# Kernel optimization log

Hardware: AMD Instinct MI355X
Metric: run time of the kernel (lower is better)

The kernel has to match this reference:

```python
import jax, jax.numpy as jnp
import numpy as np

B, D, H = 2048, 64, 512  # batch, state dim, vf hidden dim
IS_DIFFUSION = True      # vf output divided by 2.0 as in CNF.forward


def setup_inputs() -> dict:
    key = jax.random.key(0)
    ks = jax.random.split(key, 8)

    def lin(k, fi, fo):
        return jax.random.normal(k, (fi, fo), jnp.float32) / np.float32(np.sqrt(fi))

    return {
        "t": jax.random.uniform(ks[0], (1,), jnp.float32),      # scalar time, kept as [1]
        "x": jax.random.normal(ks[1], (B, D + 1), jnp.float32),  # last col = logp channel
        "W1": lin(ks[2], D + 1, H),
        "b1": jax.random.normal(ks[3], (H,), jnp.float32) * 0.01,
        "W2": lin(ks[4], H, H),
        "b2": jax.random.normal(ks[5], (H,), jnp.float32) * 0.01,
        "W3": lin(ks[6], H, D),
        "b3": jax.random.normal(ks[7], (D,), jnp.float32) * 0.01,
    }


def reference(t, x, W1, b1, W2, b2, W3, b3):
    scale = 2.0 if IS_DIFFUSION else 1.0
    xd = x[..., :-1]  # [B, D] -- drop augmented log-density channel

    def vf_single(xi):  # R^D -> R^D vector field, t and params closed over
        h = jnp.concatenate([xi, t])           # [D+1] (time-conditioned input)
        h = jnp.tanh(h @ W1 + b1)
        h = jnp.tanh(h @ W2 + b2)
        return (h @ W3 + b3) / scale

    dx = jax.vmap(vf_single)(xd)  # [B, D]
    # exact divergence: trace of per-sample Jacobian via reverse-mode (matches torch jacrev)
    div = jax.vmap(lambda xi: jnp.trace(jax.jacrev(vf_single)(xi)))(xd)  # [B]
    return jnp.concatenate([dx, div[:, None]], axis=-1)  # [B, D+1]
```

## Files before the change

### kernel.cpp

```cpp
#include <hip/hip_runtime.h>


constexpr int HD = 512;
constexpr int DD = 64;
constexpr int SB = 8;
constexpr int NB = 2048 / SB;

typedef __attribute__((ext_vector_type(8))) short bf16x8;
typedef __attribute__((ext_vector_type(4))) float f32x4;

__device__ inline unsigned short f2bf(float f) {
    union { float f; unsigned u; } v; v.f = f;
    return (unsigned short)((v.u + 0x7fffu + ((v.u >> 16) & 1u)) >> 16);
}
__device__ inline float fast_tanh(float xx) {
    float e = __expf(2.f * xx);
    return 1.f - 2.f / (e + 1.f);
}

__global__ __launch_bounds__(64) void cnf_pack_kernel(
    const float* __restrict__ W1, const float* __restrict__ W2,
    const float* __restrict__ W3, unsigned short* __restrict__ Bpack)
{
    __shared__ float w1s[64][33];
    __shared__ float w3s[16][65];
    const int b = blockIdx.x;
    const int mat = b >> 9, t = (b >> 4) & 31, kk = b & 15;
    const int l = threadIdx.x;
    const int q = l >> 4, nl = l & 15;
    const int n = t * 16 + nl;
    unsigned short o[8];
    if (mat == 0) {
#pragma unroll
        for (int j = 0; j < 8; ++j) {
            int k = kk * 32 + q * 8 + j;
            o[j] = f2bf(W2[k * HD + n]);
        }
    } else {
        for (int e = l; e < 64 * 32; e += 64) {
            int i = e >> 5, kl = e & 31;
            w1s[i][kl] = W1[i * HD + kk * 32 + kl];
        }
        for (int e = l; e < 16 * 64; e += 64) {
            int nn = e >> 6, i = e & 63;
            w3s[nn][i] = W3[(t * 16 + nn) * DD + i];
        }
        __syncthreads();
#pragma unroll
        for (int j = 0; j < 8; ++j) {
            int kl = q * 8 + j;
            float m = 0.f;
#pragma unroll 8
            for (int i = 0; i < 64; ++i) m += w1s[i][kl] * w3s[nl][i];
            o[j] = f2bf(W2[(kk * 32 + kl) * HD + n] * m);
        }
    }
    uint4 pk;
    pk.x = (unsigned)o[0] | ((unsigned)o[1] << 16);
    pk.y = (unsigned)o[2] | ((unsigned)o[3] << 16);
    pk.z = (unsigned)o[4] | ((unsigned)o[5] << 16);
    pk.w = (unsigned)o[6] | ((unsigned)o[7] << 16);
    reinterpret_cast<uint4*>(Bpack)[b * 64 + l] = pk;
}

__global__ __launch_bounds__(512) void cnf_fused_kernel(
    const float* __restrict__ tptr, const float* __restrict__ x,
    const float* __restrict__ W1, const float* __restrict__ b1,
    const float* __restrict__ b2v, const float* __restrict__ W3,
    const float* __restrict__ b3, const unsigned short* __restrict__ Bpack,
    float* __restrict__ out)
{
    __shared__ float4 xsv[65 * 2];
    __shared__ unsigned short A_lds[16][520];
    __shared__ float4 h2v[HD * 2];
    __shared__ float4 divred[8][2];
    __shared__ float sm_b2[HD];

    const int tid  = threadIdx.x;
    const int s0   = blockIdx.x * SB;
    const int wave = tid >> 6, lane = tid & 63;

    {
        const float tval = tptr[0];
        for (int e = tid; e < SB * 65; e += 512) {
            int s = e / 65, i = e % 65;
            reinterpret_cast<float*>(xsv)[i * SB + s] =
                (i == DD) ? tval : x[(s0 + s) * 65 + i];
        }
        sm_b2[tid] = b2v[tid];
    }
    __syncthreads();

    {
        const int u = tid;
        const float bb = b1[u];
        float2 a0 = {bb, bb}, a1 = {bb, bb}, a2 = {bb, bb}, a3 = {bb, bb};
        for (int ib = 0; ib < 64; ib += 8) {
            float w[8];
#pragma unroll
            for (int qq = 0; qq < 8; ++qq) w[qq] = W1[(ib + qq) * HD + u];
#pragma unroll
            for (int qq = 0; qq < 8; ++qq) {
                float4 p = xsv[2 * (ib + qq)], r = xsv[2 * (ib + qq) + 1];
                a0.x += p.x * w[qq]; a0.y += p.y * w[qq];
                a1.x += p.z * w[qq]; a1.y += p.w * w[qq];
                a2.x += r.x * w[qq]; a2.y += r.y * w[qq];
                a3.x += r.z * w[qq]; a3.y += r.w * w[qq];
            }
        }
        {
            float w = W1[64 * HD + u];
            float4 p = xsv[128], r = xsv[129];
            a0.x += p.x * w; a0.y += p.y * w;
            a1.x += p.z * w; a1.y += p.w * w;
            a2.x += r.x * w; a2.y += r.y * w;
            a3.x += r.z * w; a3.y += r.w * w;
        }
        float h[8] = {fast_tanh(a0.x), fast_tanh(a0.y), fast_tanh(a1.x), fast_tanh(a1.y),
                      fast_tanh(a2.x), fast_tanh(a2.y), fast_tanh(a3.x), fast_tanh(a3.y)};
#pragma unroll
        for (int s = 0; s < 8; ++s) {
            A_lds[s][u]     = f2bf(h[s]);
            A_lds[8 + s][u] = f2bf(1.f - h[s] * h[s]);
        }
    }
    __syncthreads();

    f32x4 cw[4], cg[4];
#pragma unroll
    for (int i = 0; i < 4; ++i) { cw[i] = (f32x4){0,0,0,0}; cg[i] = (f32x4){0,0,0,0}; }
    {
        const unsigned short* arow = &A_lds[lane & 15][0];
        const int aoff = (lane >> 4) * 8;
        const bf16x8* bw = reinterpret_cast<const bf16x8*>(Bpack)
                         + (size_t)(wave * 64) * 64 + lane;
        const bf16x8* bg = bw + 32768;
#pragma unroll 4
        for (int kk = 0; kk < 16; ++kk) {
            bf16x8 af = *reinterpret_cast<const bf16x8*>(arow + kk * 32 + aoff);
            bf16x8 w0 = bw[kk * 64],        w1f = bw[kk * 64 + 1024];
            bf16x8 w2f = bw[kk * 64 + 2048], w3f = bw[kk * 64 + 3072];
            cw[0] = __builtin_amdgcn_mfma_f32_16x16x32_bf16(af, w0,  cw[0], 0, 0, 0);
            cw[1] = __builtin_amdgcn_mfma_f32_16x16x32_bf16(af, w1f, cw[1], 0, 0, 0);
            cw[2] = __builtin_amdgcn_mfma_f32_16x16x32_bf16(af, w2f, cw[2], 0, 0, 0);
            cw[3] = __builtin_amdgcn_mfma_f32_16x16x32_bf16(af, w3f, cw[3], 0, 0, 0);
            bf16x8 g0 = bg[kk * 64],        g1f = bg[kk * 64 + 1024];
            bf16x8 g2f = bg[kk * 64 + 2048], g3f = bg[kk * 64 + 3072];
            cg[0] = __builtin_amdgcn_mfma_f32_16x16x32_bf16(af, g0,  cg[0], 0, 0, 0);
            cg[1] = __builtin_amdgcn_mfma_f32_16x16x32_bf16(af, g1f, cg[1], 0, 0, 0);
            cg[2] = __builtin_amdgcn_mfma_f32_16x16x32_bf16(af, g2f, cg[2], 0, 0, 0);
            cg[3] = __builtin_amdgcn_mfma_f32_16x16x32_bf16(af, g3f, cg[3], 0, 0, 0);
        }
    }

    {
        const int q = lane >> 4;
        const int src = (lane >= 32) ? lane - 32 : lane;
        float4 dp = {0.f, 0.f, 0.f, 0.f};
#pragma unroll
        for (int i = 0; i < 4; ++i) {
            const int m = wave * 64 + i * 16 + (lane & 15);
            const float bb = sm_b2[m];
            float4 hv;
            hv.x = fast_tanh(cw[i][0] + bb);
            hv.y = fast_tanh(cw[i][1] + bb);
            hv.z = fast_tanh(cw[i][2] + bb);
            hv.w = fast_tanh(cw[i][3] + bb);
            if (lane < 32) h2v[2 * m + q] = hv;
            float h0 = __shfl(hv.x, src), h1s = __shfl(hv.y, src);
            float h2s = __shfl(hv.z, src), h3s = __shfl(hv.w, src);
            dp.x += cg[i][0] * (1.f - h0 * h0);
            dp.y += cg[i][1] * (1.f - h1s * h1s);
            dp.z += cg[i][2] * (1.f - h2s * h2s);
            dp.w += cg[i][3] * (1.f - h3s * h3s);
        }
        if (lane >= 32) {
#pragma unroll
            for (int off = 8; off > 0; off >>= 1) {
                dp.x += __shfl_down(dp.x, off, 16);
                dp.y += __shfl_down(dp.y, off, 16);
                dp.z += __shfl_down(dp.z, off, 16);
                dp.w += __shfl_down(dp.w, off, 16);
            }
            if ((lane & 15) == 0) divred[wave][q - 2] = dp;
        }
    }
    __syncthreads();

    float* opart = reinterpret_cast<float*>(A_lds);

    {
        const int k = lane, part = wave;
        float o[8];
#pragma unroll
        for (int q = 0; q < 8; ++q) o[q] = 0.f;
        const int mb = part * 64;
        for (int mm = 0; mm < 64; mm += 4) {
            float w[4];
#pragma unroll
            for (int q = 0; q < 4; ++q) w[q] = W3[(mb + mm + q) * DD + k];
#pragma unroll
            for (int q = 0; q < 4; ++q) {
                const int m = mb + mm + q;
                float4 ha = h2v[2 * m], hb = h2v[2 * m + 1];
                o[0] += ha.x * w[q]; o[1] += ha.y * w[q];
                o[2] += ha.z * w[q]; o[3] += ha.w * w[q];
                o[4] += hb.x * w[q]; o[5] += hb.y * w[q];
                o[6] += hb.z * w[q]; o[7] += hb.w * w[q];
            }
        }
#pragma unroll
        for (int q = 0; q < 8; ++q) opart[part * 512 + q * 64 + k] = o[q];
    }
    __syncthreads();

    {
        const int s = tid >> 6, k = tid & 63;
        float sum = b3[k];
#pragma unroll
        for (int p = 0; p < 8; ++p) sum += opart[p * 512 + s * 64 + k];
        out[(s0 + s) * 65 + k] = 0.5f * sum;
    }
    if (tid < 8) {
        const int qq = tid >> 2, r = tid & 3;
        float ds = 0.f;
#pragma unroll
        for (int w = 0; w < 8; ++w)
            ds += reinterpret_cast<const float*>(&divred[w][qq])[r];
        out[(s0 + tid) * 65 + DD] = 0.5f * ds;
    }
}

extern "C" void kernel_launch(void* const* d_in, const int* in_sizes, int n_in,
                              void* d_out, int out_size, void* d_ws, size_t ws_size,
                              hipStream_t stream) {
    const float* t  = (const float*)d_in[0];
    const float* x  = (const float*)d_in[1];
    const float* W1 = (const float*)d_in[2];
    const float* b1 = (const float*)d_in[3];
    const float* W2 = (const float*)d_in[4];
    const float* b2 = (const float*)d_in[5];
    const float* W3 = (const float*)d_in[6];
    const float* b3 = (const float*)d_in[7];
    float* out = (float*)d_out;
    unsigned short* Bpack = (unsigned short*)d_ws;

    cnf_pack_kernel<<<1024, 64, 0, stream>>>(W1, W2, W3, Bpack);
    cnf_fused_kernel<<<NB, 512, 0, stream>>>(t, x, W1, b1, b2, W3, b3, Bpack, out);
}
```

Before: 102.3 us.

## Repack MFMA weights per wave and prefetch with triple-buffered registers

Changes the packed bf16 weight layout so each wave's per-k-step fragments are contiguous, then issues register prefetches of those fragments two k-steps ahead in a triple buffer, starting before the layer-1 compute. Also sets launch bounds to two blocks per SM and widens the W1 and W3 load batches to 16 and 8. The aim is to hide global-load latency of the weight stream behind the layer-1 work and the MFMAs. The cost is higher register pressure (24 bf16x8 buffers), which may conflict with the occupancy hint and cause spills.

```diff
diff --git a/kernel.cpp b/kernel.cpp
--- a/kernel.cpp
+++ b/kernel.cpp
@@ -60,10 +60,12 @@
     pk.y = (unsigned)o[2] | ((unsigned)o[3] << 16);
     pk.z = (unsigned)o[4] | ((unsigned)o[5] << 16);
     pk.w = (unsigned)o[6] | ((unsigned)o[7] << 16);
-    reinterpret_cast<uint4*>(Bpack)[b * 64 + l] = pk;
-}
-
-__global__ __launch_bounds__(512) void cnf_fused_kernel(
+    const int w = t >> 2;
+    const int t8 = mat * 4 + (t & 3);
+    reinterpret_cast<uint4*>(Bpack)[((w * 16 + kk) * 8 + t8) * 64 + l] = pk;
+}
+
+__global__ __launch_bounds__(512, 2) void cnf_fused_kernel(
     const float* __restrict__ tptr, const float* __restrict__ x,
     const float* __restrict__ W1, const float* __restrict__ b1,
     const float* __restrict__ b2v, const float* __restrict__ W3,
@@ -80,6 +82,14 @@
     const int s0   = blockIdx.x * SB;
     const int wave = tid >> 6, lane = tid & 63;
 
+    const bf16x8* bp = reinterpret_cast<const bf16x8*>(Bpack)
+                     + (size_t)wave * 8192 + lane;
+    bf16x8 buf[3][8];
+#pragma unroll
+    for (int j = 0; j < 8; ++j) buf[0][j] = bp[j * 64];
+#pragma unroll
+    for (int j = 0; j < 8; ++j) buf[1][j] = bp[512 + j * 64];
+
     {
         const float tval = tptr[0];
         for (int e = tid; e < SB * 65; e += 512) {
@@ -95,12 +105,12 @@
         const int u = tid;
         const float bb = b1[u];
         float2 a0 = {bb, bb}, a1 = {bb, bb}, a2 = {bb, bb}, a3 = {bb, bb};
-        for (int ib = 0; ib < 64; ib += 8) {
-            float w[8];
-#pragma unroll
-            for (int qq = 0; qq < 8; ++qq) w[qq] = W1[(ib + qq) * HD + u];
-#pragma unroll
-            for (int qq = 0; qq < 8; ++qq) {
+        for (int ib = 0; ib < 64; ib += 16) {
+            float w[16];
+#pragma unroll
+            for (int qq = 0; qq < 16; ++qq) w[qq] = W1[(ib + qq) * HD + u];
+#pragma unroll
+            for (int qq = 0; qq < 16; ++qq) {
                 float4 p = xsv[2 * (ib + qq)], r = xsv[2 * (ib + qq) + 1];
                 a0.x += p.x * w[qq]; a0.y += p.y * w[qq];
                 a1.x += p.z * w[qq]; a1.y += p.w * w[qq];
@@ -132,29 +142,25 @@
     {
         const unsigned short* arow = &A_lds[lane & 15][0];
         const int aoff = (lane >> 4) * 8;
-        const bf16x8* bw = reinterpret_cast<const bf16x8*>(Bpack)
-                         + (size_t)(wave * 64) * 64 + lane;
-        const bf16x8* bg = bw + 32768;
-#pragma unroll 4
+#pragma unroll
         for (int kk = 0; kk < 16; ++kk) {
+            if (kk + 2 < 16) {
+#pragma unroll
+                for (int j = 0; j < 8; ++j)
+                    buf[(kk + 2) % 3][j] = bp[(kk + 2) * 512 + j * 64];
+            }
             bf16x8 af = *reinterpret_cast<const bf16x8*>(arow + kk * 32 + aoff);
-            bf16x8 w0 = bw[kk * 64],        w1f = bw[kk * 64 + 1024];
-            bf16x8 w2f = bw[kk * 64 + 2048], w3f = bw[kk * 64 + 3072];
-            cw[0] = __builtin_amdgcn_mfma_f32_16x16x32_bf16(af, w0,  cw[0], 0, 0, 0);
-            cw[1] = __builtin_amdgcn_mfma_f32_16x16x32_bf16(af, w1f, cw[1], 0, 0, 0);
-            cw[2] = __builtin_amdgcn_mfma_f32_16x16x32_bf16(af, w2f, cw[2], 0, 0, 0);
-            cw[3] = __builtin_amdgcn_mfma_f32_16x16x32_bf16(af, w3f, cw[3], 0, 0, 0);
-            bf16x8 g0 = bg[kk * 64],        g1f = bg[kk * 64 + 1024];
-            bf16x8 g2f = bg[kk * 64 + 2048], g3f = bg[kk * 64 + 3072];
-            cg[0] = __builtin_amdgcn_mfma_f32_16x16x32_bf16(af, g0,  cg[0], 0, 0, 0);
-            cg[1] = __builtin_amdgcn_mfma_f32_16x16x32_bf16(af, g1f, cg[1], 0, 0, 0);
-            cg[2] = __builtin_amdgcn_mfma_f32_16x16x32_bf16(af, g2f, cg[2], 0, 0, 0);
-            cg[3] = __builtin_amdgcn_mfma_f32_16x16x32_bf16(af, g3f, cg[3], 0, 0, 0);
-        }
-    }
-
-    {
-        const int q = lane >> 4;
+#pragma unroll
+            for (int i = 0; i < 4; ++i)
+                cw[i] = __builtin_amdgcn_mfma_f32_16x16x32_bf16(af, buf[kk % 3][i], cw[i], 0, 0, 0);
+#pragma unroll
+            for (int i = 0; i < 4; ++i)
+                cg[i] = __builtin_amdgcn_mfma_f32_16x16x32_bf16(af, buf[kk % 3][4 + i], cg[i], 0, 0, 0);
+        }
+    }
+
+    {
+        const int qd = lane >> 4;
         const int src = (lane >= 32) ? lane - 32 : lane;
         float4 dp = {0.f, 0.f, 0.f, 0.f};
 #pragma unroll
@@ -166,7 +172,7 @@
             hv.y = fast_tanh(cw[i][1] + bb);
             hv.z = fast_tanh(cw[i][2] + bb);
             hv.w = fast_tanh(cw[i][3] + bb);
-            if (lane < 32) h2v[2 * m + q] = hv;
+            if (lane < 32) h2v[2 * m + qd] = hv;
             float h0 = __shfl(hv.x, src), h1s = __shfl(hv.y, src);
             float h2s = __shfl(hv.z, src), h3s = __shfl(hv.w, src);
             dp.x += cg[i][0] * (1.f - h0 * h0);
@@ -182,7 +188,7 @@
                 dp.z += __shfl_down(dp.z, off, 16);
                 dp.w += __shfl_down(dp.w, off, 16);
             }
-            if ((lane & 15) == 0) divred[wave][q - 2] = dp;
+            if ((lane & 15) == 0) divred[wave][qd - 2] = dp;
         }
     }
     __syncthreads();
@@ -195,12 +201,12 @@
 #pragma unroll
         for (int q = 0; q < 8; ++q) o[q] = 0.f;
         const int mb = part * 64;
-        for (int mm = 0; mm < 64; mm += 4) {
-            float w[4];
-#pragma unroll
-            for (int q = 0; q < 4; ++q) w[q] = W3[(mb + mm + q) * DD + k];
-#pragma unroll
-            for (int q = 0; q < 4; ++q) {
+        for (int mm = 0; mm < 64; mm += 8) {
+            float w[8];
+#pragma unroll
+            for (int q = 0; q < 8; ++q) w[q] = W3[(mb + mm + q) * DD + k];
+#pragma unroll
+            for (int q = 0; q < 8; ++q) {
                 const int m = mb + mm + q;
                 float4 ha = h2v[2 * m], hb = h2v[2 * m + 1];
                 o[0] += ha.x * w[q]; o[1] += ha.y * w[q];
```

Result: faster. 99.41 us (-2.9%).
